# Optimization experiments

Measured on AMD Instinct MI355X. Metric: run time of the kernel, lower is better.

## Reference

```python
import jax, jax.numpy as jnp
import numpy as np

N_NODES = 50000


def gcn_conv(x, W, b, src, dst, num_nodes):
    # x: [N, Fin] -> lin -> [N, Fout]; gather source feats per edge, scatter-add at dst.
    h = x @ W                                   # [N, Fout]
    msg = h[src]                                # [E, Fout]  (message = x_j, no edge_weight)
    out = jax.ops.segment_sum(msg, dst, num_segments=num_nodes)  # [N, Fout]
    return out + b


def setup_inputs() -> dict:
    key = jax.random.key(0)
    k1, k2, k3, k4 = jax.random.split(key, 4)
    x = jax.random.normal(k1, (N_NODES, 128), dtype=jnp.float32)
    edge_index = jax.random.randint(k2, (2, 800000), 0, N_NODES, dtype=jnp.int64)
    W1 = jax.random.normal(k3, (128, 256), dtype=jnp.float32) * (1.0 / np.sqrt(128))
    b1 = jnp.zeros((256,), dtype=jnp.float32)
    W2 = jax.random.normal(k4, (256, 40), dtype=jnp.float32) * (1.0 / np.sqrt(256))
    b2 = jnp.zeros((40,), dtype=jnp.float32)
    return {"x": x, "edge_index": edge_index, "W1": W1, "b1": b1, "W2": W2, "b2": b2}


def reference(x, edge_index, W1, b1, W2, b2):
    src, dst = edge_index[0], edge_index[1]
    h = gcn_conv(x, W1, b1, src, dst, N_NODES)
    h = jax.nn.relu(h)
    out = gcn_conv(h, W2, b2, src, dst, N_NODES)
    return out
```

## Files before the change

### kernel.cpp

```cpp
#include <hip/hip_runtime.h>

typedef unsigned int u32;
typedef unsigned short u16;
using f32x4 = __attribute__((ext_vector_type(4))) float;
using f32x2 = __attribute__((ext_vector_type(2))) float;
using s16x8 = __attribute__((ext_vector_type(8))) short;
using s16x4 = __attribute__((ext_vector_type(4))) short;

__device__ __forceinline__ u16 rne_bf16(float f) {
  u32 u = __float_as_uint(f);
  u += 0x7FFF + ((u >> 16) & 1);
  return (u16)(u >> 16);
}
__device__ __forceinline__ float bf_lo(u32 u) { return __uint_as_float(u << 16); }
__device__ __forceinline__ float bf_hi(u32 u) { return __uint_as_float(u & 0xFFFF0000u); }

#define NBX 12500
#define CAP 64
#define SCAT 2048

__global__ void zero_k(int4* __restrict__ cnt4, int nc4) {
  int i = blockIdx.x * 256 + threadIdx.x;
  if (i < nc4) cnt4[i] = make_int4(0, 0, 0, 0);
}

__global__ __launch_bounds__(256) void mega_k(const int* __restrict__ srcv,
                                              const int* __restrict__ dstv,
                                              int* __restrict__ cnt,
                                              u16* __restrict__ adj,
                                              int E, int nbin,
                                              const float* __restrict__ x, u32* __restrict__ xb,
                                              int n2,
                                              const float* __restrict__ W1, u16* __restrict__ W1t,
                                              const float* __restrict__ W2, u16* __restrict__ W2t) {
  int b = blockIdx.x, t = threadIdx.x;
  if (b < SCAT) {
    int p = b & 7;
    int lo = p * nbin, hi = lo + nbin;
    int g = b >> 3;
    int ngroups = SCAT >> 3;
    int stride = ngroups * 256;
    for (int i = g * 256 + t; i < E; i += stride) {
      int d = dstv[i];
      if (d >= lo && d < hi) {
        int pos = atomicAdd(&cnt[d], 1);
        if (pos < CAP) adj[(size_t)d * CAP + pos] = (u16)srcv[i];
      }
    }
  } else if (b < SCAT + NBX) {
    int i = (b - SCAT) * 256 + t;
    if (i < n2) {
      f32x2 v = *((const f32x2*)x + i);
      xb[i] = (u32)rne_bf16(v.x) | ((u32)rne_bf16(v.y) << 16);
    }
  } else if (b < SCAT + NBX + 128) {
    int idx = (b - SCAT - NBX) * 256 + t;
    int n = idx >> 7, k = idx & 127;
    W1t[idx] = rne_bf16(W1[k * 256 + n]);
  } else {
    int idx = (b - SCAT - NBX - 128) * 256 + t;
    int c = idx >> 8, k = idx & 255;
    W2t[idx] = (c < 40) ? rne_bf16(W2[k * 40 + c]) : (u16)0;
  }
}

__global__ void agg128_k(const u32* __restrict__ xb, const u16* __restrict__ adj,
                         const int* __restrict__ cnt, u32* __restrict__ aggb, int n) {
  int lane = threadIdx.x & 63;
  int node = blockIdx.x * 4 + (threadIdx.x >> 6);
  if (node >= n) return;
  int deg = cnt[node]; if (deg > CAP) deg = CAP;
  const u16* ab = adj + (size_t)node * CAP;
  float ax = 0.f, ay = 0.f;
  int i = 0;
  for (; i + 8 <= deg; i += 8) {
    u32 u0 = xb[(size_t)ab[i] * 64 + lane];
    u32 u1 = xb[(size_t)ab[i + 1] * 64 + lane];
    u32 u2 = xb[(size_t)ab[i + 2] * 64 + lane];
    u32 u3 = xb[(size_t)ab[i + 3] * 64 + lane];
    u32 u4 = xb[(size_t)ab[i + 4] * 64 + lane];
    u32 u5 = xb[(size_t)ab[i + 5] * 64 + lane];
    u32 u6 = xb[(size_t)ab[i + 6] * 64 + lane];
    u32 u7 = xb[(size_t)ab[i + 7] * 64 + lane];
    ax += ((bf_lo(u0) + bf_lo(u1)) + (bf_lo(u2) + bf_lo(u3)))
        + ((bf_lo(u4) + bf_lo(u5)) + (bf_lo(u6) + bf_lo(u7)));
    ay += ((bf_hi(u0) + bf_hi(u1)) + (bf_hi(u2) + bf_hi(u3)))
        + ((bf_hi(u4) + bf_hi(u5)) + (bf_hi(u6) + bf_hi(u7)));
  }
  for (; i + 2 <= deg; i += 2) {
    u32 u0 = xb[(size_t)ab[i] * 64 + lane];
    u32 u1 = xb[(size_t)ab[i + 1] * 64 + lane];
    ax += bf_lo(u0) + bf_lo(u1); ay += bf_hi(u0) + bf_hi(u1);
  }
  for (; i < deg; ++i) {
    u32 u = xb[(size_t)ab[i] * 64 + lane];
    ax += bf_lo(u); ay += bf_hi(u);
  }
  aggb[(size_t)node * 64 + lane] = (u32)rne_bf16(ax) | ((u32)rne_bf16(ay) << 16);
}

__global__ __launch_bounds__(64) void fused_k(const u16* __restrict__ Ab,
                                              const u16* __restrict__ W1t,
                                              const float* __restrict__ b1,
                                              const u16* __restrict__ W2t,
                                              u32* __restrict__ zb, int M) {
  __shared__ short slab[2][16 * 34];
  const int l = threadIdx.x;
  const int p = l & 15, g = l >> 4;
  const int m0 = blockIdx.x * 32;

  s16x8 af[2][4];
  #pragma unroll
  for (int rt = 0; rt < 2; ++rt) {
    int mrow = m0 + rt * 16 + p;
    int mload = (mrow < M) ? mrow : (M - 1);
    const u16* arow = Ab + (size_t)mload * 128 + g * 8;
    #pragma unroll
    for (int kt = 0; kt < 4; ++kt) af[rt][kt] = *(const s16x8*)(arow + kt * 32);
  }

  f32x4 acc2[2][3];
  #pragma unroll
  for (int rt = 0; rt < 2; ++rt)
    #pragma unroll
    for (int n2 = 0; n2 < 3; ++n2) acc2[rt][n2] = (f32x4){0.f, 0.f, 0.f, 0.f};

  #pragma unroll 2
  for (int s = 0; s < 8; ++s) {
    const int n0 = 2 * s, n1 = 2 * s + 1;
    const u16* w0 = W1t + (size_t)(n0 * 16 + p) * 128 + g * 8;
    const u16* w1 = W1t + (size_t)(n1 * 16 + p) * 128 + g * 8;
    s16x8 wA[4], wB[4];
    #pragma unroll
    for (int kt = 0; kt < 4; ++kt) {
      wA[kt] = *(const s16x8*)(w0 + kt * 32);
      wB[kt] = *(const s16x8*)(w1 + kt * 32);
    }
    float4 bva = *(const float4*)(b1 + n0 * 16 + g * 4);
    float4 bvb = *(const float4*)(b1 + n1 * 16 + g * 4);
    #pragma unroll
    for (int rt = 0; rt < 2; ++rt) {
      f32x4 aA = {0.f, 0.f, 0.f, 0.f};
      f32x4 aB = {0.f, 0.f, 0.f, 0.f};
      #pragma unroll
      for (int kt = 0; kt < 4; ++kt) {
        aA = __builtin_amdgcn_mfma_f32_16x16x32_bf16(wA[kt], af[rt][kt], aA, 0, 0, 0);
        aB = __builtin_amdgcn_mfma_f32_16x16x32_bf16(wB[kt], af[rt][kt], aB, 0, 0, 0);
      }
      s16x4 pa, pb;
      pa[0] = (short)rne_bf16(fmaxf(aA[0] + bva.x, 0.f));
      pa[1] = (short)rne_bf16(fmaxf(aA[1] + bva.y, 0.f));
      pa[2] = (short)rne_bf16(fmaxf(aA[2] + bva.z, 0.f));
      pa[3] = (short)rne_bf16(fmaxf(aA[3] + bva.w, 0.f));
      pb[0] = (short)rne_bf16(fmaxf(aB[0] + bvb.x, 0.f));
      pb[1] = (short)rne_bf16(fmaxf(aB[1] + bvb.y, 0.f));
      pb[2] = (short)rne_bf16(fmaxf(aB[2] + bvb.z, 0.f));
      pb[3] = (short)rne_bf16(fmaxf(aB[3] + bvb.w, 0.f));
      *(s16x4*)&slab[rt][p * 34 + g * 4] = pa;
      *(s16x4*)&slab[rt][p * 34 + 16 + g * 4] = pb;
    }
    #pragma unroll
    for (int n2 = 0; n2 < 3; ++n2) {
      s16x8 wf = *(const s16x8*)(W2t + (size_t)(n2 * 16 + p) * 256 + s * 32 + g * 8);
      #pragma unroll
      for (int rt = 0; rt < 2; ++rt) {
        s16x8 a2 = *(const s16x8*)&slab[rt][p * 34 + g * 8];
        acc2[rt][n2] = __builtin_amdgcn_mfma_f32_16x16x32_bf16(wf, a2, acc2[rt][n2], 0, 0, 0);
      }
    }
  }

  #pragma unroll
  for (int rt = 0; rt < 2; ++rt) {
    int mrow = m0 + rt * 16 + p;
    if (mrow < M) {
      #pragma unroll
      for (int n2 = 0; n2 < 3; ++n2) {
        int c0 = n2 * 16 + g * 4;
        if (c0 < 40) {
          uint2 o;
          o.x = (u32)rne_bf16(acc2[rt][n2][0]) | ((u32)rne_bf16(acc2[rt][n2][1]) << 16);
          o.y = (u32)rne_bf16(acc2[rt][n2][2]) | ((u32)rne_bf16(acc2[rt][n2][3]) << 16);
          *(uint2*)(zb + (size_t)mrow * 20 + n2 * 8 + g * 2) = o;
        }
      }
    }
  }
}

__global__ void agg40_k(const u32* __restrict__ zb, const u16* __restrict__ adj,
                        const int* __restrict__ cnt, const float* __restrict__ bias,
                        float* __restrict__ outp, int n) {
  int hl = threadIdx.x & 31;
  int node = blockIdx.x * 8 + (threadIdx.x >> 5);
  if (node >= n || hl >= 20) return;
  int deg = cnt[node]; if (deg > CAP) deg = CAP;
  const u16* ab = adj + (size_t)node * CAP;
  float ax = 0.f, ay = 0.f;
  int i = 0;
  for (; i + 4 <= deg; i += 4) {
    u32 u0 = zb[(size_t)ab[i] * 20 + hl];
    u32 u1 = zb[(size_t)ab[i + 1] * 20 + hl];
    u32 u2 = zb[(size_t)ab[i + 2] * 20 + hl];
    u32 u3 = zb[(size_t)ab[i + 3] * 20 + hl];
    ax += (bf_lo(u0) + bf_lo(u1)) + (bf_lo(u2) + bf_lo(u3));
    ay += (bf_hi(u0) + bf_hi(u1)) + (bf_hi(u2) + bf_hi(u3));
  }
  for (; i < deg; ++i) {
    u32 u = zb[(size_t)ab[i] * 20 + hl];
    ax += bf_lo(u); ay += bf_hi(u);
  }
  float2 bv = ((const float2*)bias)[hl];
  ((float2*)(outp + (size_t)node * 40))[hl] = make_float2(ax + bv.x, ay + bv.y);
}

extern "C" void kernel_launch(void* const* d_in, const int* in_sizes, int n_in,
                              void* d_out, int out_size, void* d_ws, size_t ws_size,
                              hipStream_t stream) {
  const float* x  = (const float*)d_in[0];
  const int*   ei = (const int*)d_in[1];
  const float* W1 = (const float*)d_in[2];
  const float* b1 = (const float*)d_in[3];
  const float* W2 = (const float*)d_in[4];
  const float* b2 = (const float*)d_in[5];
  float* out = (float*)d_out;

  int N = in_sizes[0] / 128;
  int E = in_sizes[1] / 2;
  const int* src = ei;
  const int* dst = ei + E;

  char* ws = (char*)d_ws;
  size_t off = 0;
  auto carve = [&](size_t bytes) {
    char* p = ws + off;
    off += (bytes + 255) & ~(size_t)255;
    return p;
  };
  u32* xb    = (u32*)carve((size_t)N * 128 * 2);
  u32* aggb  = (u32*)carve((size_t)N * 128 * 2);
  u16* W1t   = (u16*)carve(256 * 128 * 2);
  u16* W2t   = (u16*)carve(48 * 256 * 2);
  u32* zbuf  = (u32*)carve((size_t)N * 20 * 4);
  int* cnt   = (int*)carve((size_t)N * 4);
  u16* adj   = (u16*)carve((size_t)N * CAP * 2);

  int nbin = (N + 7) / 8;
  int nc4 = (N + 3) / 4;

  zero_k<<<(nc4 + 255) / 256, 256, 0, stream>>>((int4*)cnt, nc4);
  mega_k<<<SCAT + NBX + 128 + 48, 256, 0, stream>>>(src, dst, cnt, adj, E, nbin,
                                                    x, xb, N * 64, W1, W1t, W2, W2t);
  agg128_k<<<(N + 3) / 4, 256, 0, stream>>>(xb, adj, cnt, aggb, N);
  fused_k<<<(N + 31) / 32, 64, 0, stream>>>((const u16*)aggb, W1t, b1, W2t, zbuf, N);
  agg40_k<<<(N + 7) / 8, 256, 0, stream>>>(zbuf, adj, cnt, b2, out, N);
}
```

Measured before the change: 128.0 us.

## Stage W1 and W2 in padded LDS, shared by eight waves per block

The fused MLP kernel now runs 8 waves per 512-thread block instead of one 64-thread wave. Each block cooperatively copies the bf16 W1t and W2t weights into shared memory, using padded row strides to avoid bank conflicts. All waves then read weight fragments from LDS instead of re-fetching them from global memory or L2 per wave. The trade-offs are about 117KB of LDS per block, which likely limits each CU to one block, a staging pass plus barrier in every block, and only about 196 blocks launched.

```diff
diff --git a/kernel.cpp b/kernel.cpp
--- a/kernel.cpp
+++ b/kernel.cpp
@@ -18,6 +18,8 @@
 #define NBX 12500
 #define CAP 64
 #define SCAT 2048
+#define W1S 72
+#define W2S 136
 
 __global__ void zero_k(int4* __restrict__ cnt4, int nc4) {
   int i = blockIdx.x * 256 + threadIdx.x;
@@ -99,15 +101,19 @@
   aggb[(size_t)node * 64 + lane] = (u32)rne_bf16(ax) | ((u32)rne_bf16(ay) << 16);
 }
 
-__global__ __launch_bounds__(64) void fused_k(const u16* __restrict__ Ab,
-                                              const u16* __restrict__ W1t,
-                                              const float* __restrict__ b1,
-                                              const u16* __restrict__ W2t,
-                                              u32* __restrict__ zb, int M) {
-  __shared__ short slab[2][16 * 34];
-  const int l = threadIdx.x;
+__global__ __launch_bounds__(512) void fused_k(const u16* __restrict__ Ab,
+                                               const u16* __restrict__ W1t,
+                                               const float* __restrict__ b1,
+                                               const u16* __restrict__ W2t,
+                                               u32* __restrict__ zb, int M) {
+  __shared__ u32 lw1[256 * W1S];
+  __shared__ u32 lw2[48 * W2S];
+  __shared__ short slab[8][2][16 * 34];
+  const int tid = threadIdx.x;
+  const int wid = tid >> 6;
+  const int l = tid & 63;
   const int p = l & 15, g = l >> 4;
-  const int m0 = blockIdx.x * 32;
+  const int m0 = (blockIdx.x * 8 + wid) * 32;
 
   s16x8 af[2][4];
   #pragma unroll
@@ -119,6 +125,16 @@
     for (int kt = 0; kt < 4; ++kt) af[rt][kt] = *(const s16x8*)(arow + kt * 32);
   }
 
+  for (int idx = tid; idx < 16384; idx += 512) {
+    int row = idx >> 6, col = idx & 63;
+    lw1[row * W1S + col] = ((const u32*)W1t)[idx];
+  }
+  for (int idx = tid; idx < 6144; idx += 512) {
+    int row = idx >> 7, col = idx & 127;
+    lw2[row * W2S + col] = ((const u32*)W2t)[idx];
+  }
+  __syncthreads();
+
   f32x4 acc2[2][3];
   #pragma unroll
   for (int rt = 0; rt < 2; ++rt)
@@ -128,14 +144,15 @@
   #pragma unroll 2
   for (int s = 0; s < 8; ++s) {
     const int n0 = 2 * s, n1 = 2 * s + 1;
-    const u16* w0 = W1t + (size_t)(n0 * 16 + p) * 128 + g * 8;
-    const u16* w1 = W1t + (size_t)(n1 * 16 + p) * 128 + g * 8;
-    s16x8 wA[4], wB[4];
+    s16x8 wA[4], wB[4], wf[3];
     #pragma unroll
     for (int kt = 0; kt < 4; ++kt) {
-      wA[kt] = *(const s16x8*)(w0 + kt * 32);
-      wB[kt] = *(const s16x8*)(w1 + kt * 32);
-    }
+      wA[kt] = *(const s16x8*)&lw1[(n0 * 16 + p) * W1S + kt * 16 + g * 4];
+      wB[kt] = *(const s16x8*)&lw1[(n1 * 16 + p) * W1S + kt * 16 + g * 4];
+    }
+    #pragma unroll
+    for (int n2 = 0; n2 < 3; ++n2)
+      wf[n2] = *(const s16x8*)&lw2[(n2 * 16 + p) * W2S + s * 16 + g * 4];
     float4 bva = *(const float4*)(b1 + n0 * 16 + g * 4);
     float4 bvb = *(const float4*)(b1 + n1 * 16 + g * 4);
     #pragma unroll
@@ -156,16 +173,15 @@
       pb[1] = (short)rne_bf16(fmaxf(aB[1] + bvb.y, 0.f));
       pb[2] = (short)rne_bf16(fmaxf(aB[2] + bvb.z, 0.f));
       pb[3] = (short)rne_bf16(fmaxf(aB[3] + bvb.w, 0.f));
-      *(s16x4*)&slab[rt][p * 34 + g * 4] = pa;
-      *(s16x4*)&slab[rt][p * 34 + 16 + g * 4] = pb;
+      *(s16x4*)&slab[wid][rt][p * 34 + g * 4] = pa;
+      *(s16x4*)&slab[wid][rt][p * 34 + 16 + g * 4] = pb;
     }
     #pragma unroll
     for (int n2 = 0; n2 < 3; ++n2) {
-      s16x8 wf = *(const s16x8*)(W2t + (size_t)(n2 * 16 + p) * 256 + s * 32 + g * 8);
       #pragma unroll
       for (int rt = 0; rt < 2; ++rt) {
-        s16x8 a2 = *(const s16x8*)&slab[rt][p * 34 + g * 8];
-        acc2[rt][n2] = __builtin_amdgcn_mfma_f32_16x16x32_bf16(wf, a2, acc2[rt][n2], 0, 0, 0);
+        s16x8 a2 = *(const s16x8*)&slab[wid][rt][p * 34 + g * 8];
+        acc2[rt][n2] = __builtin_amdgcn_mfma_f32_16x16x32_bf16(wf[n2], a2, acc2[rt][n2], 0, 0, 0);
       }
     }
   }
@@ -252,6 +268,6 @@
   mega_k<<<SCAT + NBX + 128 + 48, 256, 0, stream>>>(src, dst, cnt, adj, E, nbin,
                                                     x, xb, N * 64, W1, W1t, W2, W2t);
   agg128_k<<<(N + 3) / 4, 256, 0, stream>>>(xb, adj, cnt, aggb, N);
-  fused_k<<<(N + 31) / 32, 64, 0, stream>>>((const u16*)aggb, W1t, b1, W2t, zbuf, N);
+  fused_k<<<(N + 255) / 256, 512, 0, stream>>>((const u16*)aggb, W1t, b1, W2t, zbuf, N);
   agg40_k<<<(N + 7) / 8, 256, 0, stream>>>(zbuf, adj, cnt, b2, out, N);
 }
```

Result: faster. 119.1 us (-6.9%).
